# Optimization experiments

Measured on AMD Instinct MI355X. Metric: run time of the kernel, lower is better.

Reference implementation:

```python
import jax, jax.numpy as jnp
import numpy as np

B, N, K, C, CM = 4, 1024, 9, 32, 128
SIGMA = 1.0
EPS = 1e-5
SLOPE = 0.01  # LeakyReLU default negative slope


def _batchnorm(x, gamma, beta):
    # training-mode BatchNorm1d over the point dimension
    m = x.mean(axis=0)
    v = x.var(axis=0)
    return gamma * (x - m) * jax.lax.rsqrt(v + EPS) + beta


def setup_inputs() -> dict:
    key = jax.random.key(0)
    ks = jax.random.split(key, 8)
    positions = jax.random.uniform(ks[0], (B * N, 2), jnp.float32) * 10.0
    weights = jax.random.normal(ks[1], (B * N, C), jnp.float32)
    # learned kernel offsets (grid-init in original; random offsets of same scale here)
    kernel_pos = jax.random.normal(ks[2], (K, 2), jnp.float32) * (2.0 * SIGMA)
    conv_w = jax.random.normal(ks[3], (K, C, C), jnp.float32) / np.sqrt(K * C)
    w1 = jax.random.normal(ks[4], (C, CM), jnp.float32) / np.sqrt(C)
    w2 = jax.random.normal(ks[5], (CM, C), jnp.float32) / np.sqrt(CM)
    return {
        "positions": positions,
        "weights": weights,
        "kernel_pos": kernel_pos,
        "conv_w": conv_w,
        "bn_gamma": jnp.ones((C,), jnp.float32),
        "bn_beta": jnp.zeros((C,), jnp.float32),
        "w1": w1,
        "b1": jnp.zeros((CM,), jnp.float32),
        "bn1_gamma": jnp.ones((CM,), jnp.float32),
        "bn1_beta": jnp.zeros((CM,), jnp.float32),
        "w2": w2,
        "b2": jnp.zeros((C,), jnp.float32),
        "n_batch": B,
        "n_points": N,
    }


def reference(positions, weights, kernel_pos, conv_w, bn_gamma, bn_beta,
              w1, b1, bn1_gamma, bn1_beta, w2, b2, n_batch, n_points):
    b, n = n_batch, n_points
    k = kernel_pos.shape[0]
    c = weights.shape[-1]
    pos = positions.reshape(b, n, 2)
    w = weights.reshape(b, n, c)

    # KernelConv: each component spawns K shifted components with channel mixing
    comp_pos = pos[:, :, None, :] + kernel_pos[None, None, :, :]      # [b,n,k,2]
    comp_w = jnp.einsum('bnc,kcd->bnkd', w, conv_w)                   # [b,n,k,c]

    # KernelSample: evaluate the resulting Gaussian mixture at the input positions
    diff = pos[:, :, None, None, :] - comp_pos[:, None, :, :, :]      # [b,i,n,k,2]
    dist2 = jnp.sum(diff * diff, axis=-1)                             # [b,i,n,k]
    kmat = jnp.exp(-dist2 / (2.0 * SIGMA * SIGMA))
    y = jnp.einsum('bink,bnkc->bic', kmat, comp_w)                    # [b,i,c]
    y = jax.nn.leaky_relu(y, SLOPE)
    y = y.reshape(b * n, c)

    # conv_norm + residual add of input weights
    y = _batchnorm(y, bn_gamma, bn_beta)
    y = y + weights

    # PyG MLP [C, CM, C], act_first=True, plain_last=True
    h = y @ w1 + b1
    h = jax.nn.leaky_relu(h, SLOPE)
    h = _batchnorm(h, bn1_gamma, bn1_beta)
    delta = h @ w2 + b2

    return y + delta  # output weights [b*n, c]; positions pass through unchanged
```

## Files before the change

### kernel.cpp

```cpp
#include <hip/hip_runtime.h>

#define BB 4
#define NN 1024
#define KK 9
#define C  32
#define CM 128
#define M  (BB*NN)
#define EPSB 1e-5f
#define SLOPE 0.01f

#define SCH 4
#define NCH 256
#define NSUB 32
#define KDIM 288
#define KPAD 296
#define CHUNK_F16 (32*KPAD)

typedef _Float16 f16x8 __attribute__((ext_vector_type(8)));
typedef _Float16 f16x4 __attribute__((ext_vector_type(4)));
typedef float    f32x4 __attribute__((ext_vector_type(4)));

__device__ __forceinline__ float leaky(float x){ return x > 0.f ? x : SLOPE*x; }

__global__ __launch_bounds__(256) void k1_compw(const float* __restrict__ w,
                                                const float* __restrict__ conv_w,
                                                _Float16* __restrict__ cwh,
                                                float* __restrict__ stats){
  __shared__ float cwl[3*C*C];
  int bid = blockIdx.x;
  int kt  = bid % 3;
  int sub = (bid/3)&7, nc = (bid/24)&3, b = bid/96;
  int tid = threadIdx.x;
  if (bid == 0){ for (int i = tid; i < 320; i += 256) stats[i] = 0.f; }

  const float4* cs = (const float4*)(conv_w + kt*3*C*C);
  float4* cd = (float4*)cwl;
  for (int v = tid; v < 768; v += 256) cd[v] = cs[v];

  int nl = tid & 31, dq = tid >> 5;
  int row = ((b*4 + nc)*8 + sub)*32 + nl;
  float wreg[32];
  const float4* wr = (const float4*)(w + (size_t)row*C);
  #pragma unroll
  for (int j = 0; j < 8; ++j){
    float4 t = wr[j];
    wreg[4*j]=t.x; wreg[4*j+1]=t.y; wreg[4*j+2]=t.z; wreg[4*j+3]=t.w;
  }
  __syncthreads();

  _Float16* outb = cwh + (size_t)((b*4+nc)*8 + sub)*CHUNK_F16;
  const float4* cv = (const float4*)cwl;
  #pragma unroll
  for (int kl = 0; kl < 3; ++kl){
    float a0=0.f, a1=0.f, a2=0.f, a3=0.f;
    #pragma unroll
    for (int c = 0; c < C; ++c){
      float4 t = cv[kl*256 + c*8 + dq];
      a0 += wreg[c]*t.x; a1 += wreg[c]*t.y; a2 += wreg[c]*t.z; a3 += wreg[c]*t.w;
    }
    int k = kt*3 + kl;
    outb[(dq*4+0)*KPAD + k*32 + nl] = (_Float16)a0;
    outb[(dq*4+1)*KPAD + k*32 + nl] = (_Float16)a1;
    outb[(dq*4+2)*KPAD + k*32 + nl] = (_Float16)a2;
    outb[(dq*4+3)*KPAD + k*32 + nl] = (_Float16)a3;
  }
}

__global__ __launch_bounds__(256) void k2_main(const float* __restrict__ pos,
                                               const float* __restrict__ kpos,
                                               const _Float16* __restrict__ cwh,
                                               float* __restrict__ part){
  __shared__ _Float16 km[32*KPAD];
  __shared__ _Float16 cw[32*KPAD];
  __shared__ float pnl[NCH*2];
  int bid = blockIdx.x;
  int nc = bid & 3, it = (bid>>2)&31, b = bid>>7;
  int tid = threadIdx.x;
  int lane = tid & 63, wid = tid >> 6;
  int i0 = (wid>>1)*16, c0 = (wid&1)*16;
  int mm = lane & 15, quad = lane >> 4;

  const float* pbase = pos + (size_t)(b*NN + nc*NCH)*2;
  for (int v = tid; v < NCH*2; v += 256) pnl[v] = pbase[v];

  int ig = tid >> 3, np = tid & 7;
  float pix = pos[(size_t)(b*NN + it*32 + ig)*2];
  float piy = pos[(size_t)(b*NN + it*32 + ig)*2 + 1];
  float kx[KK], ky[KK];
  #pragma unroll
  for (int k = 0; k < KK; ++k){ kx[k] = kpos[2*k]; ky[k] = kpos[2*k+1]; }

  f32x4 acc = {0.f,0.f,0.f,0.f};
  __syncthreads();

  for (int s = 0; s < 8; ++s){
    const float4* srcs = (const float4*)(cwh + (size_t)((b*4+nc)*8 + s)*CHUNK_F16);
    float4* dst = (float4*)cw;
    for (int v = tid; v < CHUNK_F16/8; v += 256) dst[v] = srcs[v];

    float dx[4], dy[4];
    #pragma unroll
    for (int jj = 0; jj < 4; ++jj){
      int nl = np*4 + jj;
      dx[jj] = pix - pnl[2*(s*32+nl)];
      dy[jj] = piy - pnl[2*(s*32+nl)+1];
    }
    #pragma unroll
    for (int k = 0; k < KK; ++k){
      f16x4 ev;
      #pragma unroll
      for (int jj = 0; jj < 4; ++jj){
        float ddx = dx[jj]-kx[k], ddy = dy[jj]-ky[k];
        ev[jj] = (_Float16)__expf(-0.5f*(ddx*ddx + ddy*ddy));
      }
      *(f16x4*)&km[ig*KPAD + k*32 + np*4] = ev;
    }
    __syncthreads();

    #pragma unroll
    for (int ks = 0; ks < 9; ++ks){
      f16x8 a  = *(const f16x8*)&km[(i0+mm)*KPAD + ks*32 + quad*8];
      f16x8 bf = *(const f16x8*)&cw[(c0+mm)*KPAD + ks*32 + quad*8];
      acc = __builtin_amdgcn_mfma_f32_16x16x32_f16(a, bf, acc, 0, 0, 0);
    }
    __syncthreads();
  }

  int grow0 = b*NN + it*32 + i0;
  #pragma unroll
  for (int r = 0; r < 4; ++r){
    int grow = grow0 + quad*4 + r;
    part[((size_t)nc*M + grow)*C + c0 + mm] = acc[r];
  }
}

__global__ __launch_bounds__(256) void k3_reduce(const float* __restrict__ part,
                                                 float* __restrict__ z,
                                                 float* __restrict__ stats,
                                                 int S){
  __shared__ float ls1[C], ls2[C];
  int tid = threadIdx.x;
  if (tid < C){ ls1[tid]=0.f; ls2[tid]=0.f; }
  __syncthreads();
  size_t idx = (size_t)blockIdx.x*256 + tid;
  float s = 0.f;
  for (int p = 0; p < S; ++p) s += part[(size_t)p*M*C + idx];
  s = leaky(s);
  z[idx] = s;
  atomicAdd(&ls1[tid & (C-1)], s);
  atomicAdd(&ls2[tid & (C-1)], s*s);
  __syncthreads();
  if (tid < C){ atomicAdd(&stats[tid], ls1[tid]); atomicAdd(&stats[C+tid], ls2[tid]); }
}

__global__ __launch_bounds__(256) void k4_mlp1(const float* __restrict__ z,
                                               const float* __restrict__ weights,
                                               const float* __restrict__ bn_g,
                                               const float* __restrict__ bn_b,
                                               const float* __restrict__ w1,
                                               const float* __restrict__ b1,
                                               float* __restrict__ stats,
                                               float* __restrict__ y,
                                               float* __restrict__ h){
  __shared__ float w1l[C*CM];
  __shared__ float yl[16*C];
  __shared__ float lt1[CM], lt2[CM];
  int tid = threadIdx.x;
  int row0 = blockIdx.x * 16;
  for (int i = tid; i < C*CM; i += 256) w1l[i] = w1[i];
  if (tid < CM){ lt1[tid]=0.f; lt2[tid]=0.f; }
  #pragma unroll
  for (int j = 0; j < 2; ++j){
    int e = tid + j*256;
    int c  = e & (C-1);
    int rl = e >> 5;
    float s1 = stats[c], s2 = stats[C + c];
    float mean = s1 * (1.f/M);
    float var  = s2 * (1.f/M) - mean*mean;
    float sc = bn_g[c] * rsqrtf(var + EPSB);
    float sh = bn_b[c] - mean*sc;
    int row = row0 + rl;
    float v = z[(size_t)row*C + c]*sc + sh + weights[(size_t)row*C + c];
    yl[e] = v;
    y[(size_t)row*C + c] = v;
  }
  __syncthreads();
  #pragma unroll
  for (int j = 0; j < 8; ++j){
    int e = tid + j*256;
    int col = e & (CM-1);
    int rl  = e >> 7;
    float acc = b1[col];
    #pragma unroll
    for (int c = 0; c < C; ++c) acc += yl[rl*C + c] * w1l[c*CM + col];
    acc = leaky(acc);
    h[(size_t)(row0+rl)*CM + col] = acc;
    atomicAdd(&lt1[col], acc);
    atomicAdd(&lt2[col], acc*acc);
  }
  __syncthreads();
  if (tid < CM){
    atomicAdd(&stats[2*C + tid],      lt1[tid]);
    atomicAdd(&stats[2*C + CM + tid], lt2[tid]);
  }
}

__global__ __launch_bounds__(256) void k5_mlp2(const float* __restrict__ h,
                                               const float* __restrict__ y,
                                               const float* __restrict__ bn1_g,
                                               const float* __restrict__ bn1_b,
                                               const float* __restrict__ w2,
                                               const float* __restrict__ b2,
                                               const float* __restrict__ stats,
                                               float* __restrict__ out){
  __shared__ float w2l[CM*C];
  __shared__ float hl[16*CM];
  int tid = threadIdx.x;
  int row0 = blockIdx.x * 16;
  for (int i = tid; i < CM*C; i += 256) w2l[i] = w2[i];
  #pragma unroll
  for (int j = 0; j < 8; ++j){
    int e = tid + j*256;
    int col = e & (CM-1);
    int rl  = e >> 7;
    float t1 = stats[2*C + col], t2 = stats[2*C + CM + col];
    float mean = t1*(1.f/M);
    float var  = t2*(1.f/M) - mean*mean;
    float sc = bn1_g[col]*rsqrtf(var + EPSB);
    float sh = bn1_b[col] - mean*sc;
    hl[e] = h[(size_t)(row0+rl)*CM + col]*sc + sh;
  }
  __syncthreads();
  #pragma unroll
  for (int j = 0; j < 2; ++j){
    int e = tid + j*256;
    int c  = e & (C-1);
    int rl = e >> 5;
    float acc = b2[c];
    #pragma unroll
    for (int jj = 0; jj < CM; ++jj) acc += hl[rl*CM + jj] * w2l[jj*C + c];
    int row = row0 + rl;
    out[(size_t)row*C + c] = y[(size_t)row*C + c] + acc;
  }
}

extern "C" void kernel_launch(void* const* d_in, const int* in_sizes, int n_in,
                              void* d_out, int out_size, void* d_ws, size_t ws_size,
                              hipStream_t stream) {
  const float* positions = (const float*)d_in[0];
  const float* weights   = (const float*)d_in[1];
  const float* kpos      = (const float*)d_in[2];
  const float* conv_w    = (const float*)d_in[3];
  const float* bn_g      = (const float*)d_in[4];
  const float* bn_b      = (const float*)d_in[5];
  const float* w1        = (const float*)d_in[6];
  const float* b1        = (const float*)d_in[7];
  const float* bn1_g     = (const float*)d_in[8];
  const float* bn1_b     = (const float*)d_in[9];
  const float* w2        = (const float*)d_in[10];
  const float* b2        = (const float*)d_in[11];
  float* out = (float*)d_out;

  float* ws = (float*)d_ws;
  size_t off = 0;
  _Float16* cwh = (_Float16*)(ws + off); off += (size_t)128*CHUNK_F16/2;
  float* part  = ws + off; off += (size_t)SCH*M*C;
  float* z     = ws + off; off += (size_t)M*C;
  float* y     = ws + off; off += (size_t)M*C;
  float* h     = ws + off; off += (size_t)M*CM;
  float* stats = ws + off; off += 320;

  k1_compw<<<384, 256, 0, stream>>>(weights, conv_w, cwh, stats);
  k2_main <<<512, 256, 0, stream>>>(positions, kpos, cwh, part);
  k3_reduce<<<(M*C)/256, 256, 0, stream>>>(part, z, stats, SCH);
  k4_mlp1<<<M/16, 256, 0, stream>>>(z, weights, bn_g, bn_b, w1, b1, stats, y, h);
  k5_mlp2<<<M/16, 256, 0, stream>>>(h, y, bn1_g, bn1_b, w2, b2, stats, out);
}
```

Measured before the change: 149.0 us.

## Fuse split-N reduction into main kernel with double-buffered async LDS staging

Replaces the split-N main kernel plus separate reduction kernel with one kernel per 16-row tile that loops over all 1024 source points. Each workgroup computes a full output tile and applies the activation and BatchNorm statistics in-kernel. The comp_w chunks are double-buffered through global_load_lds, and generation of the next Gaussian tile overlaps the current MFMA step. The Gaussian exponent is rewritten as an exp2 of a linear form with precomputed per-kernel coefficients. The partial-sum buffer and one launch go away, at the cost of fewer workgroups (256) and a longer serial loop per block, where the nine MFMA k-steps are split across wave pairs.

```diff
diff --git a/kernel.cpp b/kernel.cpp
--- a/kernel.cpp
+++ b/kernel.cpp
@@ -9,18 +9,23 @@
 #define EPSB 1e-5f
 #define SLOPE 0.01f
 
-#define SCH 4
-#define NCH 256
-#define NSUB 32
-#define KDIM 288
 #define KPAD 296
 #define CHUNK_F16 (32*KPAD)
+#define CHUNK_F4  (CHUNK_F16/8)
 
 typedef _Float16 f16x8 __attribute__((ext_vector_type(8)));
 typedef _Float16 f16x4 __attribute__((ext_vector_type(4)));
 typedef float    f32x4 __attribute__((ext_vector_type(4)));
 
 __device__ __forceinline__ float leaky(float x){ return x > 0.f ? x : SLOPE*x; }
+
+__device__ __forceinline__ float fexp2(float x){
+#if __has_builtin(__builtin_amdgcn_exp2f)
+  return __builtin_amdgcn_exp2f(x);
+#else
+  return exp2f(x);
+#endif
+}
 
 __global__ __launch_bounds__(256) void k1_compw(const float* __restrict__ w,
                                                 const float* __restrict__ conv_w,
@@ -29,7 +34,7 @@
   __shared__ float cwl[3*C*C];
   int bid = blockIdx.x;
   int kt  = bid % 3;
-  int sub = (bid/3)&7, nc = (bid/24)&3, b = bid/96;
+  int s   = (bid/3) & 31, b = bid/96;
   int tid = threadIdx.x;
   if (bid == 0){ for (int i = tid; i < 320; i += 256) stats[i] = 0.f; }
 
@@ -38,7 +43,7 @@
   for (int v = tid; v < 768; v += 256) cd[v] = cs[v];
 
   int nl = tid & 31, dq = tid >> 5;
-  int row = ((b*4 + nc)*8 + sub)*32 + nl;
+  int row = (b*32 + s)*32 + nl;
   float wreg[32];
   const float4* wr = (const float4*)(w + (size_t)row*C);
   #pragma unroll
@@ -48,7 +53,7 @@
   }
   __syncthreads();
 
-  _Float16* outb = cwh + (size_t)((b*4+nc)*8 + sub)*CHUNK_F16;
+  _Float16* outb = cwh + (size_t)(b*32 + s)*CHUNK_F16;
   const float4* cv = (const float4*)cwl;
   #pragma unroll
   for (int kl = 0; kl < 3; ++kl){
@@ -66,91 +71,109 @@
   }
 }
 
-__global__ __launch_bounds__(256) void k2_main(const float* __restrict__ pos,
-                                               const float* __restrict__ kpos,
-                                               const _Float16* __restrict__ cwh,
-                                               float* __restrict__ part){
-  __shared__ _Float16 km[32*KPAD];
-  __shared__ _Float16 cw[32*KPAD];
-  __shared__ float pnl[NCH*2];
+__global__ __launch_bounds__(512, 2) void k2_full(const float* __restrict__ pos,
+                                                  const float* __restrict__ kpos,
+                                                  const _Float16* __restrict__ cwh,
+                                                  float* __restrict__ z,
+                                                  float* __restrict__ stats){
+  __shared__ __align__(16) _Float16 cwt[2][32*KPAD];
+  __shared__ __align__(16) _Float16 kmt[2][16*KPAD];
+  __shared__ __align__(16) float pnl[NN*2];
+  float* red  = (float*)&cwt[0][0];
+  float* red2 = (float*)&cwt[1][0];
+
   int bid = blockIdx.x;
-  int nc = bid & 3, it = (bid>>2)&31, b = bid>>7;
+  int b = bid >> 6, it = bid & 63;
   int tid = threadIdx.x;
   int lane = tid & 63, wid = tid >> 6;
-  int i0 = (wid>>1)*16, c0 = (wid&1)*16;
   int mm = lane & 15, quad = lane >> 4;
-
-  const float* pbase = pos + (size_t)(b*NN + nc*NCH)*2;
-  for (int v = tid; v < NCH*2; v += 256) pnl[v] = pbase[v];
-
-  int ig = tid >> 3, np = tid & 7;
-  float pix = pos[(size_t)(b*NN + it*32 + ig)*2];
-  float piy = pos[(size_t)(b*NN + it*32 + ig)*2 + 1];
-  float kx[KK], ky[KK];
-  #pragma unroll
-  for (int k = 0; k < KK; ++k){ kx[k] = kpos[2*k]; ky[k] = kpos[2*k+1]; }
+  int c0 = (wid & 1) * 16, q = wid >> 1;
+  int ig = tid >> 5, nl = tid & 31;
+
+  const float BETA = -0.72134752f;
+  float Ak[KK], Bk[KK], Ck[KK];
+  #pragma unroll
+  for (int k = 0; k < KK; ++k){
+    float kxx = kpos[2*k], kyy = kpos[2*k+1];
+    Ak[k] = -2.f*BETA*kxx;
+    Bk[k] = -2.f*BETA*kyy;
+    Ck[k] = BETA*(kxx*kxx + kyy*kyy);
+  }
+
+#define STAGE(dstbuf, ss) do{ \
+    const float4* s4_ = (const float4*)(cwh + (size_t)(b*32 + (ss))*CHUNK_F16); \
+    _Pragma("unroll") \
+    for (int rr_ = 0; rr_ < 3; ++rr_){ \
+      int v_ = tid + rr_*512; \
+      if (v_ < CHUNK_F4) \
+        __builtin_amdgcn_global_load_lds( \
+          (const __attribute__((address_space(1))) unsigned int*)(s4_ + v_), \
+          (__attribute__((address_space(3))) unsigned int*)((dstbuf) + (size_t)(rr_*512 + wid*64)*8), \
+          16, 0, 0); \
+    } \
+  }while(0)
+
+#define GEN(dstbuf, ss) do{ \
+    float dx_ = pix - pnl[2*((ss)*32 + nl)]; \
+    float dy_ = piy - pnl[2*((ss)*32 + nl) + 1]; \
+    float e0_ = BETA*(dx_*dx_ + dy_*dy_); \
+    _Float16* kr_ = (dstbuf) + ig*KPAD + nl; \
+    _Pragma("unroll") \
+    for (int k = 0; k < KK; ++k){ \
+      float t_ = (e0_ + Ck[k]) + dx_*Ak[k] + dy_*Bk[k]; \
+      kr_[k*32] = (_Float16)fexp2(t_); \
+    } \
+  }while(0)
+
+  ((float4*)pnl)[tid] = ((const float4*)(pos + (size_t)b*NN*2))[tid];
+  STAGE(cwt[0], 0);
+  __syncthreads();
+  float pix = pnl[2*(it*16 + ig)];
+  float piy = pnl[2*(it*16 + ig) + 1];
+  GEN(kmt[0], 0);
+  __syncthreads();
 
   f32x4 acc = {0.f,0.f,0.f,0.f};
-  __syncthreads();
-
-  for (int s = 0; s < 8; ++s){
-    const float4* srcs = (const float4*)(cwh + (size_t)((b*4+nc)*8 + s)*CHUNK_F16);
-    float4* dst = (float4*)cw;
-    for (int v = tid; v < CHUNK_F16/8; v += 256) dst[v] = srcs[v];
-
-    float dx[4], dy[4];
-    #pragma unroll
-    for (int jj = 0; jj < 4; ++jj){
-      int nl = np*4 + jj;
-      dx[jj] = pix - pnl[2*(s*32+nl)];
-      dy[jj] = piy - pnl[2*(s*32+nl)+1];
+  for (int s = 0; s < 32; ++s){
+    int cur = s & 1, nxt = cur ^ 1;
+    if (s < 31) STAGE(cwt[nxt], s+1);
+    #pragma unroll
+    for (int t = 0; t < 3; ++t){
+      int ks = q + t*4;
+      if (ks < KK){
+        f16x8 a  = *(const f16x8*)&kmt[cur][mm*KPAD + ks*32 + quad*8];
+        f16x8 bf = *(const f16x8*)&cwt[cur][(c0+mm)*KPAD + ks*32 + quad*8];
+        acc = __builtin_amdgcn_mfma_f32_16x16x32_f16(a, bf, acc, 0, 0, 0);
+      }
     }
-    #pragma unroll
-    for (int k = 0; k < KK; ++k){
-      f16x4 ev;
-      #pragma unroll
-      for (int jj = 0; jj < 4; ++jj){
-        float ddx = dx[jj]-kx[k], ddy = dy[jj]-ky[k];
-        ev[jj] = (_Float16)__expf(-0.5f*(ddx*ddx + ddy*ddy));
-      }
-      *(f16x4*)&km[ig*KPAD + k*32 + np*4] = ev;
-    }
+    if (s < 31) GEN(kmt[nxt], s+1);
     __syncthreads();
-
-    #pragma unroll
-    for (int ks = 0; ks < 9; ++ks){
-      f16x8 a  = *(const f16x8*)&km[(i0+mm)*KPAD + ks*32 + quad*8];
-      f16x8 bf = *(const f16x8*)&cw[(c0+mm)*KPAD + ks*32 + quad*8];
-      acc = __builtin_amdgcn_mfma_f32_16x16x32_f16(a, bf, acc, 0, 0, 0);
-    }
-    __syncthreads();
-  }
-
-  int grow0 = b*NN + it*32 + i0;
-  #pragma unroll
-  for (int r = 0; r < 4; ++r){
-    int grow = grow0 + quad*4 + r;
-    part[((size_t)nc*M + grow)*C + c0 + mm] = acc[r];
-  }
-}
-
-__global__ __launch_bounds__(256) void k3_reduce(const float* __restrict__ part,
-                                                 float* __restrict__ z,
-                                                 float* __restrict__ stats,
-                                                 int S){
-  __shared__ float ls1[C], ls2[C];
-  int tid = threadIdx.x;
-  if (tid < C){ ls1[tid]=0.f; ls2[tid]=0.f; }
-  __syncthreads();
-  size_t idx = (size_t)blockIdx.x*256 + tid;
-  float s = 0.f;
-  for (int p = 0; p < S; ++p) s += part[(size_t)p*M*C + idx];
-  s = leaky(s);
-  z[idx] = s;
-  atomicAdd(&ls1[tid & (C-1)], s);
-  atomicAdd(&ls2[tid & (C-1)], s*s);
-  __syncthreads();
-  if (tid < C){ atomicAdd(&stats[tid], ls1[tid]); atomicAdd(&stats[C+tid], ls2[tid]); }
+  }
+#undef STAGE
+#undef GEN
+
+  float* rp = red + wid*256;
+  #pragma unroll
+  for (int r = 0; r < 4; ++r) rp[(quad*4 + r)*16 + mm] = acc[r];
+  __syncthreads();
+  {
+    int r = tid >> 5, c = tid & 31;
+    int half = c >> 4, cc = c & 15;
+    int o = r*16 + cc;
+    float v = red[half*256 + o] + red[(2+half)*256 + o]
+            + red[(4+half)*256 + o] + red[(6+half)*256 + o];
+    v = leaky(v);
+    z[((size_t)b*NN + it*16 + r)*C + c] = v;
+    red2[c*17 + r] = v;
+  }
+  __syncthreads();
+  if (tid < C){
+    float s1 = 0.f, s2 = 0.f;
+    #pragma unroll
+    for (int r = 0; r < 16; ++r){ float t = red2[tid*17 + r]; s1 += t; s2 += t*t; }
+    atomicAdd(&stats[tid], s1);
+    atomicAdd(&stats[C + tid], s2);
+  }
 }
 
 __global__ __launch_bounds__(256) void k4_mlp1(const float* __restrict__ z,
@@ -264,15 +287,13 @@
   float* ws = (float*)d_ws;
   size_t off = 0;
   _Float16* cwh = (_Float16*)(ws + off); off += (size_t)128*CHUNK_F16/2;
-  float* part  = ws + off; off += (size_t)SCH*M*C;
   float* z     = ws + off; off += (size_t)M*C;
   float* y     = ws + off; off += (size_t)M*C;
   float* h     = ws + off; off += (size_t)M*CM;
   float* stats = ws + off; off += 320;
 
   k1_compw<<<384, 256, 0, stream>>>(weights, conv_w, cwh, stats);
-  k2_main <<<512, 256, 0, stream>>>(positions, kpos, cwh, part);
-  k3_reduce<<<(M*C)/256, 256, 0, stream>>>(part, z, stats, SCH);
-  k4_mlp1<<<M/16, 256, 0, stream>>>(z, weights, bn_g, bn_b, w1, b1, stats, y, h);
-  k5_mlp2<<<M/16, 256, 0, stream>>>(h, y, bn1_g, bn1_b, w2, b2, stats, out);
-}
+  k2_full <<<256, 512, 0, stream>>>(positions, kpos, cwh, z, stats);
+  k4_mlp1 <<<M/16, 256, 0, stream>>>(z, weights, bn_g, bn_b, w1, b1, stats, y, h);
+  k5_mlp2 <<<M/16, 256, 0, stream>>>(h, y, bn1_g, bn1_b, w2, b2, stats, out);
+}
```

New measurement: 144.1 us. -3.3%, faster.
